# Kernel tuning notes

Measured on AMD Instinct MI355X. Metric: run time of the kernel, lower is better.

The kernel has to match this reference:

```python
import jax, jax.numpy as jnp
import numpy as np

B, CIN, G, H, HW, WMIX = 128, 64, 8, 14, 16, 16  # batch, in-ch, groups, spatial, mixed width


def setup_inputs() -> dict:
    key = jax.random.key(0)
    k1, k2, k3 = jax.random.split(key, 3)
    x = jax.random.normal(k1, (B, CIN, G, H, H), dtype=jnp.float32)
    w_conv = jax.random.normal(k2, (G, 3, 3, 32), dtype=jnp.float32)   # weights[0]
    w_mix = jax.random.normal(k3, (CIN, WMIX), dtype=jnp.float32)       # weights[1]
    return {"x": x, "w_conv": w_conv, "w_mix": w_mix}


def _unfold3(t, axis, size):
    # torch F.unfold with kernel (3,1), padding (1,0) along `axis`: zero-pad by 1
    # and stack the 3 shifted windows as a new axis inserted at `axis`.
    pad = [(0, 0)] * t.ndim
    pad[axis] = (1, 1)
    p = jnp.pad(t, pad)
    slices = []
    for k in range(3):
        idx = [slice(None)] * t.ndim
        idx[axis] = slice(k, k + size)
        slices.append(p[tuple(idx)])
    return jnp.stack(slices, axis=axis)


def reference(x, w_conv, w_mix):
    # channel mix: (B, 64, 8, 14, 14) x (64, 16) -> (B, 8, 14, 14, 16)
    t4 = jnp.einsum('kjmnl,ji->kmnli', x, w_mix)
    # first unfold along H (axis 3): (B, 8, 14, 3, 14, 16)
    u1 = _unfold3(t4, 3, H)
    # second unfold along H (now axis 4): (B, 8, 14, 3, 3, 14, 16)
    u2 = _unfold3(u1, 4, H)
    # permute (0,1,2,5,4,3,6) -> (B, 8, 14, 14, 3, 3, 16)
    t5 = jnp.transpose(u2, (0, 1, 2, 5, 4, 3, 6))
    # conv channel mix: contract group(8) and both 3-taps -> (B, 14, 14, 16, 32)
    t6 = jnp.einsum('mlonikp,likj->monpj', t5, w_conv)
    # (B, 14, 14, 32, 16) -> (B, 14, 14, 512)
    t7 = jnp.transpose(t6, (0, 1, 2, 4, 3)).reshape(B, H, H, 512)
    t7 = jnp.roll(t7, 1, axis=1)  # shift_direction fixed to +1
    return jnp.transpose(t7, (0, 3, 1, 2))  # (B, 512, 14, 14)
```

## Files before the change

kernel.cpp:

```cpp
#include <hip/hip_runtime.h>

static constexpr int NB   = 128;
static constexpr int NCIN = 64;
static constexpr int NG   = 8;
static constexpr int NH   = 14;
static constexpr int NP   = 16;
static constexpr int NJ   = 32;
static constexpr int HH   = NH * NH;
static constexpr int LROW = 20;

__global__ __launch_bounds__(64) void mix_kernel(const float* __restrict__ x,
                                                 const float* __restrict__ wmix,
                                                 float* __restrict__ t4) {
    int t     = blockIdx.x * 64 + threadIdx.x;
    int squad = t % 49;
    int bg    = t / 49;
    int b     = bg >> 3;
    int g     = bg & 7;

    float acc[4][NP];
#pragma unroll
    for (int q = 0; q < 4; q++)
#pragma unroll
        for (int p = 0; p < NP; p++) acc[q][p] = 0.f;

    const float* xbase = x + (size_t)b * (NCIN * NG * HH) + (size_t)g * HH + squad * 4;

#pragma unroll 4
    for (int j = 0; j < NCIN; j++) {
        float4 xv = *reinterpret_cast<const float4*>(xbase + (size_t)j * (NG * HH));
#pragma unroll
        for (int p = 0; p < NP; p++) {
            float w = wmix[j * NP + p];
            acc[0][p] += xv.x * w;
            acc[1][p] += xv.y * w;
            acc[2][p] += xv.z * w;
            acc[3][p] += xv.w * w;
        }
    }

    float* tb = t4 + ((size_t)bg * HH + squad * 4) * NP;
#pragma unroll
    for (int q = 0; q < 4; q++)
#pragma unroll
        for (int p4 = 0; p4 < 4; p4++) {
            *reinterpret_cast<float4*>(tb + q * NP + p4 * 4) =
                make_float4(acc[q][p4 * 4 + 0], acc[q][p4 * 4 + 1],
                            acc[q][p4 * 4 + 2], acc[q][p4 * 4 + 3]);
        }
}

__global__ __launch_bounds__(128) void conv_kernel(const float* __restrict__ t4,
                                                   const float* __restrict__ wconv,
                                                   float* __restrict__ out) {
    __shared__ __align__(16) float lds[512 * 15];
    float* t4s = lds;
    float* w2s = lds + 2560;
    float* wcs = lds + 3840;

    const int tid   = threadIdx.x;
    const int b     = blockIdx.x / NH;
    const int o     = blockIdx.x % NH;
    const int o_src = (o + NH - 1) % NH;

    const float* tsl = t4 + ((size_t)b * NG * HH + (size_t)o_src * NH) * NP;
#pragma unroll
    for (int r = 0; r < 14; r++) {
        int idx = r * 128 + tid;
        int g   = idx / 224;
        int rem = idx % 224;
        int l   = rem / 16;
        int p   = rem % 16;
        t4s[(g * 16 + p) * LROW + (l + 2)] = tsl[(size_t)g * HH * NP + l * 16 + p];
    }
#pragma unroll
    for (int r = 0; r < 6; r++) {
        int idx = r * 128 + tid;
        int gp  = idx / 6;
        int s   = idx % 6;
        int l2  = (s < 2) ? s : (14 + s);
        t4s[gp * LROW + l2] = 0.f;
    }
#pragma unroll
    for (int r = 0; r < 10; r++) {
        int idx = r * 128 + tid;
        int g   = idx / 160;
        int di  = (idx / 32) % 5;
        int j   = idx % 32;
        int ilo = di > 2 ? di - 2 : 0;
        int ihi = di < 2 ? di : 2;
        float s = 0.f;
        for (int i = ilo; i <= ihi; i++) {
            int k = di - i;
            s += wconv[((g * 3 + i) * 3 + k) * 32 + j];
        }
        w2s[idx] = s;
    }
#pragma unroll
    for (int r = 0; r < 4; r++) {
        int idx = r * 128 + tid;
        int sel = idx / 256;
        int g   = (idx / 32) % 8;
        int j   = idx % 32;
        wcs[idx] = wconv[(g * 9 + (sel ? 6 : 2)) * 32 + j];
    }
    __syncthreads();

    const int p     = tid & 15;
    const int jg    = tid >> 4;
    const int jbase = jg * 4;

    float acc[NH][4];
#pragma unroll
    for (int n = 0; n < NH; n++) {
        acc[n][0] = 0.f; acc[n][1] = 0.f; acc[n][2] = 0.f; acc[n][3] = 0.f;
    }

    for (int g = 0; g < NG; g++) {
        float row[LROW];
        const float* rp = &t4s[(g * 16 + p) * LROW];
#pragma unroll
        for (int q = 0; q < 5; q++) {
            float4 v = *reinterpret_cast<const float4*>(rp + q * 4);
            row[q * 4 + 0] = v.x; row[q * 4 + 1] = v.y;
            row[q * 4 + 2] = v.z; row[q * 4 + 3] = v.w;
        }
#pragma unroll
        for (int di = 0; di < 5; di++) {
            float4 w = *reinterpret_cast<const float4*>(&w2s[(g * 5 + di) * 32 + jbase]);
#pragma unroll
            for (int n = 0; n < NH; n++) {
                float rv = row[n + di];
                acc[n][0] += rv * w.x;
                acc[n][1] += rv * w.y;
                acc[n][2] += rv * w.z;
                acc[n][3] += rv * w.w;
            }
        }
        float4 c0 = *reinterpret_cast<const float4*>(&wcs[g * 32 + jbase]);
        float4 c1 = *reinterpret_cast<const float4*>(&wcs[256 + g * 32 + jbase]);
        float r2 = row[2], r15 = row[15];
        acc[0][0]  -= r2  * c0.x; acc[0][1]  -= r2  * c0.y;
        acc[0][2]  -= r2  * c0.z; acc[0][3]  -= r2  * c0.w;
        acc[13][0] -= r15 * c1.x; acc[13][1] -= r15 * c1.y;
        acc[13][2] -= r15 * c1.z; acc[13][3] -= r15 * c1.w;
    }

    __syncthreads();

#pragma unroll
    for (int jj = 0; jj < 4; jj++) {
        int c = (jbase + jj) * 16 + p;
#pragma unroll
        for (int n = 0; n < NH; n++) lds[c * 15 + n] = acc[n][jj];
    }
    __syncthreads();

    float* ob = out + (size_t)b * 512 * HH + (size_t)o * NH;
#pragma unroll
    for (int r = 0; r < 56; r++) {
        int idx = r * 128 + tid;
        int c   = idx / 14;
        int n   = idx % 14;
        ob[(size_t)c * HH + n] = lds[c * 15 + n];
    }
}

extern "C" void kernel_launch(void* const* d_in, const int* in_sizes, int n_in,
                              void* d_out, int out_size, void* d_ws, size_t ws_size,
                              hipStream_t stream) {
    const float* x     = (const float*)d_in[0];
    const float* wconv = (const float*)d_in[1];
    const float* wmix  = (const float*)d_in[2];
    float* out = (float*)d_out;
    float* t4  = (float*)d_ws;

    mix_kernel<<<784, 64, 0, stream>>>(x, wmix, t4);
    conv_kernel<<<NB * NH, 128, 0, stream>>>(t4, wconv, out);
}
```

Before: 161.1 us.

## Fuse channel-mix into conv kernel and split output rows across two half-blocks

Removes the separate mix kernel and its intermediate t4 buffer in global memory. Each conv block now computes its own slice of the channel mix directly from x into LDS, using wmix staged in shared memory. Block size doubles to 256 so each thread handles 7 output positions instead of 14, which lowers register pressure and raises parallelism. The cost is that x rows are read per block with small float2 loads, which may be less coalesced.

```diff
diff --git a/kernel.cpp b/kernel.cpp
--- a/kernel.cpp
+++ b/kernel.cpp
@@ -5,161 +5,151 @@
 static constexpr int NG   = 8;
 static constexpr int NH   = 14;
 static constexpr int NP   = 16;
-static constexpr int NJ   = 32;
 static constexpr int HH   = NH * NH;
 static constexpr int LROW = 20;
 
-__global__ __launch_bounds__(64) void mix_kernel(const float* __restrict__ x,
-                                                 const float* __restrict__ wmix,
-                                                 float* __restrict__ t4) {
-    int t     = blockIdx.x * 64 + threadIdx.x;
-    int squad = t % 49;
-    int bg    = t / 49;
-    int b     = bg >> 3;
-    int g     = bg & 7;
-
-    float acc[4][NP];
-#pragma unroll
-    for (int q = 0; q < 4; q++)
-#pragma unroll
-        for (int p = 0; p < NP; p++) acc[q][p] = 0.f;
-
-    const float* xbase = x + (size_t)b * (NCIN * NG * HH) + (size_t)g * HH + squad * 4;
-
-#pragma unroll 4
-    for (int j = 0; j < NCIN; j++) {
-        float4 xv = *reinterpret_cast<const float4*>(xbase + (size_t)j * (NG * HH));
-#pragma unroll
-        for (int p = 0; p < NP; p++) {
-            float w = wmix[j * NP + p];
-            acc[0][p] += xv.x * w;
-            acc[1][p] += xv.y * w;
-            acc[2][p] += xv.z * w;
-            acc[3][p] += xv.w * w;
-        }
-    }
-
-    float* tb = t4 + ((size_t)bg * HH + squad * 4) * NP;
-#pragma unroll
-    for (int q = 0; q < 4; q++)
-#pragma unroll
-        for (int p4 = 0; p4 < 4; p4++) {
-            *reinterpret_cast<float4*>(tb + q * NP + p4 * 4) =
-                make_float4(acc[q][p4 * 4 + 0], acc[q][p4 * 4 + 1],
-                            acc[q][p4 * 4 + 2], acc[q][p4 * 4 + 3]);
-        }
-}
-
-__global__ __launch_bounds__(128) void conv_kernel(const float* __restrict__ t4,
-                                                   const float* __restrict__ wconv,
-                                                   float* __restrict__ out) {
+__global__ __launch_bounds__(256, 4) void fused_kernel(const float* __restrict__ x,
+                                                       const float* __restrict__ wconv,
+                                                       const float* __restrict__ wmix,
+                                                       float* __restrict__ out) {
     __shared__ __align__(16) float lds[512 * 15];
-    float* t4s = lds;
-    float* w2s = lds + 2560;
-    float* wcs = lds + 3840;
+    float* t4s   = lds;
+    float* wmixs = lds + 2560;
+    float* w2s   = lds + 3584;
+    float* wcs   = lds + 4864;
 
     const int tid   = threadIdx.x;
     const int b     = blockIdx.x / NH;
     const int o     = blockIdx.x % NH;
     const int o_src = (o + NH - 1) % NH;
 
-    const float* tsl = t4 + ((size_t)b * NG * HH + (size_t)o_src * NH) * NP;
 #pragma unroll
-    for (int r = 0; r < 14; r++) {
-        int idx = r * 128 + tid;
-        int g   = idx / 224;
-        int rem = idx % 224;
-        int l   = rem / 16;
-        int p   = rem % 16;
-        t4s[(g * 16 + p) * LROW + (l + 2)] = tsl[(size_t)g * HH * NP + l * 16 + p];
+    for (int r = 0; r < 4; r++) {
+        int idx = r * 256 + tid;
+        wmixs[idx] = wmix[idx];
     }
 #pragma unroll
-    for (int r = 0; r < 6; r++) {
-        int idx = r * 128 + tid;
-        int gp  = idx / 6;
-        int s   = idx % 6;
-        int l2  = (s < 2) ? s : (14 + s);
-        t4s[gp * LROW + l2] = 0.f;
-    }
-#pragma unroll
-    for (int r = 0; r < 10; r++) {
-        int idx = r * 128 + tid;
+    for (int r = 0; r < 5; r++) {
+        int idx = r * 256 + tid;
         int g   = idx / 160;
         int di  = (idx / 32) % 5;
         int j   = idx % 32;
         int ilo = di > 2 ? di - 2 : 0;
         int ihi = di < 2 ? di : 2;
         float s = 0.f;
-        for (int i = ilo; i <= ihi; i++) {
-            int k = di - i;
-            s += wconv[((g * 3 + i) * 3 + k) * 32 + j];
-        }
+        for (int i = ilo; i <= ihi; i++) s += wconv[((g * 3 + i) * 3 + (di - i)) * 32 + j];
         w2s[idx] = s;
     }
 #pragma unroll
-    for (int r = 0; r < 4; r++) {
-        int idx = r * 128 + tid;
+    for (int r = 0; r < 2; r++) {
+        int idx = r * 256 + tid;
         int sel = idx / 256;
         int g   = (idx / 32) % 8;
         int j   = idx % 32;
         wcs[idx] = wconv[(g * 9 + (sel ? 6 : 2)) * 32 + j];
     }
+#pragma unroll
+    for (int r = 0; r < 3; r++) {
+        int idx = r * 256 + tid;
+        int gp  = idx / 6;
+        int s   = idx % 6;
+        int l2  = (s < 2) ? s : (14 + s);
+        t4s[gp * LROW + l2] = 0.f;
+    }
     __syncthreads();
 
-    const int p     = tid & 15;
-    const int jg    = tid >> 4;
-    const int jbase = jg * 4;
+    {
+        const int lq = tid & 3;
+        const int pp = (tid >> 2) & 7;
+        const int g  = tid >> 5;
 
-    float acc[NH][4];
+        float acc[2][4];
 #pragma unroll
-    for (int n = 0; n < NH; n++) {
-        acc[n][0] = 0.f; acc[n][1] = 0.f; acc[n][2] = 0.f; acc[n][3] = 0.f;
+        for (int pi = 0; pi < 2; pi++)
+#pragma unroll
+            for (int li = 0; li < 4; li++) acc[pi][li] = 0.f;
+
+        const float* xb = x + (size_t)b * (NCIN * NG * HH) + (size_t)g * HH
+                            + o_src * NH + lq * 4;
+        const bool full = (lq < 3);
+
+#pragma unroll 4
+        for (int cin = 0; cin < NCIN; cin++) {
+            const float* xp = xb + (size_t)cin * (NG * HH);
+            float2 va = *reinterpret_cast<const float2*>(xp);
+            float2 vb = full ? *reinterpret_cast<const float2*>(xp + 2)
+                             : make_float2(0.f, 0.f);
+            float2 w = *reinterpret_cast<const float2*>(&wmixs[cin * NP + pp * 2]);
+            acc[0][0] += va.x * w.x;  acc[0][1] += va.y * w.x;
+            acc[0][2] += vb.x * w.x;  acc[0][3] += vb.y * w.x;
+            acc[1][0] += va.x * w.y;  acc[1][1] += va.y * w.y;
+            acc[1][2] += vb.x * w.y;  acc[1][3] += vb.y * w.y;
+        }
+        const int nl = full ? 4 : 2;
+#pragma unroll
+        for (int pi = 0; pi < 2; pi++)
+            for (int li = 0; li < nl; li++)
+                t4s[(g * NP + pp * 2 + pi) * LROW + 2 + lq * 4 + li] = acc[pi][li];
+    }
+    __syncthreads();
+
+    const int p  = tid & 15;
+    const int jg = (tid >> 4) & 7;
+    const int h  = tid >> 7;
+
+    float acc[7][4];
+#pragma unroll
+    for (int nn = 0; nn < 7; nn++) {
+        acc[nn][0] = 0.f; acc[nn][1] = 0.f; acc[nn][2] = 0.f; acc[nn][3] = 0.f;
     }
 
     for (int g = 0; g < NG; g++) {
-        float row[LROW];
-        const float* rp = &t4s[(g * 16 + p) * LROW];
+        float rowbuf[16];
+        const float* rp = &t4s[(g * NP + p) * LROW + 4 * h];
 #pragma unroll
-        for (int q = 0; q < 5; q++) {
+        for (int q = 0; q < 4; q++) {
             float4 v = *reinterpret_cast<const float4*>(rp + q * 4);
-            row[q * 4 + 0] = v.x; row[q * 4 + 1] = v.y;
-            row[q * 4 + 2] = v.z; row[q * 4 + 3] = v.w;
+            rowbuf[q * 4 + 0] = v.x; rowbuf[q * 4 + 1] = v.y;
+            rowbuf[q * 4 + 2] = v.z; rowbuf[q * 4 + 3] = v.w;
         }
 #pragma unroll
         for (int di = 0; di < 5; di++) {
-            float4 w = *reinterpret_cast<const float4*>(&w2s[(g * 5 + di) * 32 + jbase]);
+            float4 w = *reinterpret_cast<const float4*>(&w2s[(g * 5 + di) * 32 + jg * 4]);
 #pragma unroll
-            for (int n = 0; n < NH; n++) {
-                float rv = row[n + di];
-                acc[n][0] += rv * w.x;
-                acc[n][1] += rv * w.y;
-                acc[n][2] += rv * w.z;
-                acc[n][3] += rv * w.w;
+            for (int nn = 0; nn < 7; nn++) {
+                float rv = rowbuf[3 * h + nn + di];
+                acc[nn][0] += rv * w.x;
+                acc[nn][1] += rv * w.y;
+                acc[nn][2] += rv * w.z;
+                acc[nn][3] += rv * w.w;
             }
         }
-        float4 c0 = *reinterpret_cast<const float4*>(&wcs[g * 32 + jbase]);
-        float4 c1 = *reinterpret_cast<const float4*>(&wcs[256 + g * 32 + jbase]);
-        float r2 = row[2], r15 = row[15];
-        acc[0][0]  -= r2  * c0.x; acc[0][1]  -= r2  * c0.y;
-        acc[0][2]  -= r2  * c0.z; acc[0][3]  -= r2  * c0.w;
-        acc[13][0] -= r15 * c1.x; acc[13][1] -= r15 * c1.y;
-        acc[13][2] -= r15 * c1.z; acc[13][3] -= r15 * c1.w;
+        if (h == 0) {
+            float4 c0 = *reinterpret_cast<const float4*>(&wcs[g * 32 + jg * 4]);
+            float r0 = rowbuf[2];
+            acc[0][0] -= r0 * c0.x; acc[0][1] -= r0 * c0.y;
+            acc[0][2] -= r0 * c0.z; acc[0][3] -= r0 * c0.w;
+        } else {
+            float4 c1 = *reinterpret_cast<const float4*>(&wcs[256 + g * 32 + jg * 4]);
+            float r13 = rowbuf[11];
+            acc[6][0] -= r13 * c1.x; acc[6][1] -= r13 * c1.y;
+            acc[6][2] -= r13 * c1.z; acc[6][3] -= r13 * c1.w;
+        }
     }
-
     __syncthreads();
 
 #pragma unroll
     for (int jj = 0; jj < 4; jj++) {
-        int c = (jbase + jj) * 16 + p;
+        int c = (jg * 4 + jj) * NP + p;
 #pragma unroll
-        for (int n = 0; n < NH; n++) lds[c * 15 + n] = acc[n][jj];
+        for (int nn = 0; nn < 7; nn++) lds[c * 15 + h * 7 + nn] = acc[nn][jj];
     }
     __syncthreads();
 
     float* ob = out + (size_t)b * 512 * HH + (size_t)o * NH;
 #pragma unroll
-    for (int r = 0; r < 56; r++) {
-        int idx = r * 128 + tid;
+    for (int r = 0; r < 28; r++) {
+        int idx = r * 256 + tid;
         int c   = idx / 14;
         int n   = idx % 14;
         ob[(size_t)c * HH + n] = lds[c * 15 + n];
@@ -173,8 +163,6 @@
     const float* wconv = (const float*)d_in[1];
     const float* wmix  = (const float*)d_in[2];
     float* out = (float*)d_out;
-    float* t4  = (float*)d_ws;
 
-    mix_kernel<<<784, 64, 0, stream>>>(x, wmix, t4);
-    conv_kernel<<<NB * NH, 128, 0, stream>>>(t4, wconv, out);
+    fused_kernel<<<NB * NH, 256, 0, stream>>>(x, wconv, wmix, out);
 }
```

Result: slower. 523.5 us (+224.8%).
